# Kernel tuning notes

Measured on AMD Instinct MI355X. Metric: run time of the kernel, lower is better.

Reference implementation:

```python
import jax, jax.numpy as jnp
import numpy as np

GRID = 10
C_IN = 4          # input_dim // (grid*grid) = 400 // 100
HID = 128         # lstm hidden_dim
NV = 6            # num_vehicles
PH = 10           # pred_horizon
BN_EPS = 1e-5


def setup_inputs() -> dict:
    key = jax.random.key(0)
    ks = jax.random.split(key, 20)
    def n(k, shape, scale=0.05):
        return jax.random.normal(k, shape, jnp.float32) * scale
    return {
        "observations": jax.random.normal(ks[0], (1024, 32, 400), jnp.float32),
        # CNN
        "conv1_w": n(ks[1], (16, C_IN, 3, 3)), "conv1_b": n(ks[2], (16,)),
        "conv2_w": n(ks[3], (32, 16, 3, 3)), "conv2_b": n(ks[4], (32,)),
        # FCN (BatchNorm in eval mode: running stats + affine)
        "fc1_w": n(ks[5], (128, 128)), "fc1_b": n(ks[6], (128,)),
        "bn1_gamma": jnp.ones((128,), jnp.float32), "bn1_beta": jnp.zeros((128,), jnp.float32),
        "bn1_mean": jnp.zeros((128,), jnp.float32), "bn1_var": jnp.ones((128,), jnp.float32),
        "fc2_w": n(ks[7], (64, 128)), "fc2_b": n(ks[8], (64,)),
        "bn2_gamma": jnp.ones((64,), jnp.float32), "bn2_beta": jnp.zeros((64,), jnp.float32),
        "bn2_mean": jnp.zeros((64,), jnp.float32), "bn2_var": jnp.ones((64,), jnp.float32),
        # encoder LSTM (torch gate order i,f,g,o; b = b_ih + b_hh fused)
        "enc_w_ih": n(ks[9], (4 * HID, 64)), "enc_w_hh": n(ks[10], (4 * HID, HID)),
        "enc_b": n(ks[11], (4 * HID,)),
        # decoder LSTM
        "dec_w_ih": n(ks[12], (4 * HID, HID)), "dec_w_hh": n(ks[13], (4 * HID, HID)),
        "dec_b": n(ks[14], (4 * HID,)),
        # output head
        "out_w": n(ks[15], (2 * NV, HID)), "out_b": n(ks[16], (2 * NV,)),
    }


def _conv(x, w, b):
    y = jax.lax.conv_general_dilated(x, w, (1, 1), "SAME",
                                     dimension_numbers=("NCHW", "OIHW", "NCHW"))
    return y + b[None, :, None, None]


def _maxpool2(x):
    # MaxPool2d(2,2) with floor (drops odd trailing row/col) == VALID
    return jax.lax.reduce_window(x, -jnp.inf, jax.lax.max, (1, 1, 2, 2), (1, 1, 2, 2), "VALID")


def _bn(x, g, b, m, v):
    return (x - m) * jax.lax.rsqrt(v + BN_EPS) * g + b


def _lstm_cell(x, h, c, w_ih, w_hh, b):
    gates = x @ w_ih.T + h @ w_hh.T + b
    i, f, g, o = jnp.split(gates, 4, axis=-1)
    c_new = jax.nn.sigmoid(f) * c + jax.nn.sigmoid(i) * jnp.tanh(g)
    h_new = jax.nn.sigmoid(o) * jnp.tanh(c_new)
    return h_new, c_new


def reference(observations, conv1_w, conv1_b, conv2_w, conv2_b,
              fc1_w, fc1_b, bn1_gamma, bn1_beta, bn1_mean, bn1_var,
              fc2_w, fc2_b, bn2_gamma, bn2_beta, bn2_mean, bn2_var,
              enc_w_ih, enc_w_hh, enc_b, dec_w_ih, dec_w_hh, dec_b,
              out_w, out_b):
    B, T, D = observations.shape
    # ---- fuse the per-frame Python loop: batch all B*T frames at once ----
    x = observations.reshape(B * T, C_IN, GRID, GRID)
    x = _maxpool2(jax.nn.relu(_conv(x, conv1_w, conv1_b)))   # [BT,16,5,5]
    x = _maxpool2(jax.nn.relu(_conv(x, conv2_w, conv2_b)))   # [BT,32,2,2]
    x = x.reshape(B * T, -1)                                 # [BT,128]
    x = jax.nn.relu(_bn(x @ fc1_w.T + fc1_b, bn1_gamma, bn1_beta, bn1_mean, bn1_var))
    x = jax.nn.relu(_bn(x @ fc2_w.T + fc2_b, bn2_gamma, bn2_beta, bn2_mean, bn2_var))
    feats = x.reshape(B, T, 64)

    # ---- encoder LSTM ----
    h0 = jnp.zeros((B, HID), feats.dtype)
    c0 = jnp.zeros((B, HID), feats.dtype)
    def enc_step(carry, xt):
        h, c = carry
        h, c = _lstm_cell(xt, h, c, enc_w_ih, enc_w_hh, enc_b)
        return (h, c), h
    (h_n, c_n), hs = jax.lax.scan(enc_step, (h0, c0), jnp.swapaxes(feats, 0, 1))
    dec_x = hs[-1]  # encoder_output[:, -1]

    def dec_step(carry, _):
        x_in, h, c = carry
        h, c = _lstm_cell(x_in, h, c, dec_w_ih, dec_w_hh, dec_b)
        pred = h @ out_w.T + out_b
        return (h, h, c), pred
    _, preds = jax.lax.scan(dec_step, (dec_x, h_n, c_n), None, length=PH)
    return jnp.swapaxes(preds, 0, 1)  # [B, PH, 2*NV]
```

## Files before the change

### kernel.cpp

```cpp
#include <hip/hip_runtime.h>
#include <hip/hip_bf16.h>
#include <hip/hip_fp16.h>

constexpr int GT = 32768;
constexpr int TSEQ = 32;

typedef _Float16 h2 __attribute__((ext_vector_type(2)));

#if defined(__has_builtin)
#if __has_builtin(__builtin_amdgcn_fdot2)
#define FDOT2(a, b, c) __builtin_amdgcn_fdot2((a), (b), (c), false)
#endif
#endif
#ifndef FDOT2
#define FDOT2(a, b, c) fmaf((float)(a).x, (float)(b).x, fmaf((float)(a).y, (float)(b).y, (c)))
#endif

__device__ __forceinline__ h2 pack2(float a, float b) {
  h2 v; v.x = (_Float16)a; v.y = (_Float16)b; return v;
}

constexpr size_t OBS_T  = 0;
constexpr size_t POOL1H = 13107200;
constexpr size_t POOL2H = 0;
constexpr size_t Y1H    = 2097152;
constexpr size_t FEATSH = 19660800;
constexpr size_t GX     = 0;
constexpr size_t WB     = 26214400;
constexpr size_t W_C1   = WB + 0;
constexpr size_t W_C2H  = WB + 576;
constexpr size_t W_F1H  = WB + 2880;
constexpr size_t B_F1   = WB + 11072;
constexpr size_t W_F2H  = WB + 11200;
constexpr size_t B_F2   = WB + 15296;
constexpr size_t W_ENCXH= WB + 15360;
constexpr size_t W_ENCHH= WB + 31744;
constexpr size_t B_ENC  = WB + 64512;
constexpr size_t W_DECH = WB + 65024;
constexpr size_t B_DEC  = WB + 97792;

__device__ __forceinline__ float sigf(float x)  { return 1.f / (1.f + __expf(-x)); }
__device__ __forceinline__ float tanhfast(float x) { return 1.f - 2.f / (__expf(2.f * x) + 1.f); }

__global__ __launch_bounds__(256) void k_setup(
    const float* __restrict__ c1w, const float* __restrict__ c2w,
    const float* __restrict__ f1w, const float* __restrict__ f1b,
    const float* __restrict__ g1, const float* __restrict__ be1,
    const float* __restrict__ m1, const float* __restrict__ v1,
    const float* __restrict__ f2w, const float* __restrict__ f2b,
    const float* __restrict__ g2, const float* __restrict__ be2,
    const float* __restrict__ m2, const float* __restrict__ v2,
    const float* __restrict__ ewih, const float* __restrict__ ewhh, const float* __restrict__ eb,
    const float* __restrict__ dwih, const float* __restrict__ dwhh, const float* __restrict__ db,
    float* __restrict__ ws) {
  h2* wsh = (h2*)ws;
  long i = (long)blockIdx.x * 256 + threadIdx.x;
  if (i < 576)  { int c = i & 15, r = i >> 4; ws[W_C1 + i] = c1w[c * 36 + r]; return; }
  i -= 576;
  if (i < 2304) { int co = i & 31, q = i >> 5; int ci2 = q / 9, t9 = q % 9;
    wsh[W_C2H + i] = pack2(c2w[co * 144 + (2 * ci2) * 9 + t9],
                           c2w[co * 144 + (2 * ci2 + 1) * 9 + t9]); return; }
  i -= 2304;
  if (i < 8192) { int j = i & 127, q = i >> 7; int co2 = q >> 2, pos = q & 3;
    float s = g1[j] * rsqrtf(v1[j] + 1e-5f);
    wsh[W_F1H + i] = pack2(f1w[j * 128 + 8 * co2 + pos] * s,
                           f1w[j * 128 + 8 * co2 + 4 + pos] * s); return; }
  i -= 8192;
  if (i < 128) { int j = i; float s = g1[j] * rsqrtf(v1[j] + 1e-5f);
    ws[B_F1 + i] = (f1b[j] - m1[j]) * s + be1[j]; return; }
  i -= 128;
  if (i < 4096) { int j = i & 63, k2 = i >> 6;
    float s = g2[j] * rsqrtf(v2[j] + 1e-5f);
    wsh[W_F2H + i] = pack2(f2w[j * 128 + 2 * k2] * s,
                           f2w[j * 128 + 2 * k2 + 1] * s); return; }
  i -= 4096;
  if (i < 64) { int j = i; float s = g2[j] * rsqrtf(v2[j] + 1e-5f);
    ws[B_F2 + i] = (f2b[j] - m2[j]) * s + be2[j]; return; }
  i -= 64;
  if (i < 16384) { int r = i & 511, k2 = i >> 9;
    int u = r >> 2, gt = r & 3, jr = gt * 128 + u;
    wsh[W_ENCXH + i] = pack2(ewih[jr * 64 + 2 * k2], ewih[jr * 64 + 2 * k2 + 1]); return; }
  i -= 16384;
  if (i < 32768) { int r = i & 511, k2 = i >> 9;
    int u = r >> 2, gt = r & 3, jr = gt * 128 + u;
    wsh[W_ENCHH + i] = pack2(ewhh[jr * 128 + 2 * k2], ewhh[jr * 128 + 2 * k2 + 1]); return; }
  i -= 32768;
  if (i < 512) { int u = i >> 2, gt = i & 3; ws[B_ENC + i] = eb[gt * 128 + u]; return; }
  i -= 512;
  if (i < 32768) { int r = i & 511, k2 = i >> 9;
    int u = r >> 2, gt = r & 3, jr = gt * 128 + u;
    wsh[W_DECH + i] = pack2(dwih[jr * 128 + 2 * k2] + dwhh[jr * 128 + 2 * k2],
                            dwih[jr * 128 + 2 * k2 + 1] + dwhh[jr * 128 + 2 * k2 + 1]); return; }
  i -= 32768;
  if (i < 512) { int u = i >> 2, gt = i & 3; ws[B_DEC + i] = db[gt * 128 + u]; return; }
}

__global__ __launch_bounds__(256) void k_transpose(const float* __restrict__ obs,
                                                   float* __restrict__ obsT) {
  __shared__ float tile[64][65];
  int tp0 = blockIdx.x * 64;
  int b0  = blockIdx.y * 64;
  int q     = threadIdx.x & 15;
  int rbase = threadIdx.x >> 4;
  #pragma unroll
  for (int rr = 0; rr < 4; ++rr) {
    int row = rbase + rr * 16;
    const float4 v = *(const float4*)(obs + (size_t)(b0 + row) * 12800 + tp0 + q * 4);
    tile[row][q * 4 + 0] = v.x;
    tile[row][q * 4 + 1] = v.y;
    tile[row][q * 4 + 2] = v.z;
    tile[row][q * 4 + 3] = v.w;
  }
  __syncthreads();
  int lane = threadIdx.x & 63;
  int grp  = threadIdx.x >> 6;
  for (int cc = 0; cc < 16; ++cc) {
    int col = grp * 16 + cc;
    int tp = tp0 + col;
    int t = tp / 400, p = tp % 400;
    obsT[(size_t)p * GT + t * 1024 + b0 + lane] = tile[lane][col];
  }
}

__global__ __launch_bounds__(256) void k_conv1(const float* __restrict__ obsT,
                                               const float* __restrict__ wT,
                                               const float* __restrict__ bias,
                                               h2* __restrict__ pool1h) {
  int g = blockIdx.x * 256 + threadIdx.x;
  int pos = blockIdx.y;
  int py = pos / 5, px = pos % 5;
  float acc[4][16];
  #pragma unroll
  for (int s = 0; s < 4; ++s)
    #pragma unroll
    for (int c = 0; c < 16; ++c) acc[s][c] = 0.f;

  #pragma unroll 1
  for (int ci = 0; ci < 4; ++ci) {
    float p[16];
    #pragma unroll
    for (int r = 0; r < 4; ++r) {
      int iy = 2 * py + r - 1;
      #pragma unroll
      for (int cx = 0; cx < 4; ++cx) {
        int ix = 2 * px + cx - 1;
        bool ok = ((unsigned)iy < 10u) && ((unsigned)ix < 10u);
        p[r * 4 + cx] = ok ? obsT[(size_t)(ci * 100 + iy * 10 + ix) * GT + g] : 0.f;
      }
    }
    #pragma unroll
    for (int t9 = 0; t9 < 9; ++t9) {
      int ky = t9 / 3, kx = t9 % 3;
      const float* w = wT + ((ci * 9 + t9) << 4);
      float wv[16];
      #pragma unroll
      for (int c = 0; c < 16; ++c) wv[c] = w[c];
      #pragma unroll
      for (int dy = 0; dy < 2; ++dy)
        #pragma unroll
        for (int dx = 0; dx < 2; ++dx) {
          float xv = p[(dy + ky) * 4 + (dx + kx)];
          #pragma unroll
          for (int c = 0; c < 16; ++c)
            acc[dy * 2 + dx][c] = fmaf(wv[c], xv, acc[dy * 2 + dx][c]);
        }
    }
  }
  float m[16];
  #pragma unroll
  for (int c = 0; c < 16; ++c) {
    float v = fmaxf(fmaxf(acc[0][c], acc[1][c]), fmaxf(acc[2][c], acc[3][c]));
    m[c] = fmaxf(v + bias[c], 0.f);
  }
  #pragma unroll
  for (int c2 = 0; c2 < 8; ++c2)
    pool1h[(size_t)(c2 * 25 + pos) * GT + g] = pack2(m[2 * c2], m[2 * c2 + 1]);
}

__global__ __launch_bounds__(256) void k_conv2h(const h2* __restrict__ pool1h,
                                                const h2* __restrict__ wch,
                                                const float* __restrict__ bias,
                                                h2* __restrict__ pool2h) {
  int g = blockIdx.x * 256 + threadIdx.x;
  int pos = blockIdx.y & 3;
  int h = blockIdx.y >> 2;
  int py = pos >> 1, px = pos & 1;
  float acc[4][8];
  #pragma unroll
  for (int s = 0; s < 4; ++s)
    #pragma unroll
    for (int c = 0; c < 8; ++c) acc[s][c] = 0.f;
  const h2 hz = pack2(0.f, 0.f);

  #pragma unroll 1
  for (int ci2 = 0; ci2 < 8; ++ci2) {
    h2 p[16];
    #pragma unroll
    for (int r = 0; r < 4; ++r) {
      int iy = 2 * py + r - 1;
      #pragma unroll
      for (int cx = 0; cx < 4; ++cx) {
        int ix = 2 * px + cx - 1;
        bool ok = ((unsigned)iy < 5u) && ((unsigned)ix < 5u);
        p[r * 4 + cx] = ok ? pool1h[(size_t)(ci2 * 25 + iy * 5 + ix) * GT + g] : hz;
      }
    }
    #pragma unroll
    for (int t9 = 0; t9 < 9; ++t9) {
      int ky = t9 / 3, kx = t9 % 3;
      const h2* w = wch + (ci2 * 9 + t9) * 32 + h * 8;
      h2 wv[8];
      #pragma unroll
      for (int c = 0; c < 8; ++c) wv[c] = w[c];
      #pragma unroll
      for (int dy = 0; dy < 2; ++dy)
        #pragma unroll
        for (int dx = 0; dx < 2; ++dx) {
          h2 xv = p[(dy + ky) * 4 + (dx + kx)];
          #pragma unroll
          for (int c = 0; c < 8; ++c)
            acc[dy * 2 + dx][c] = FDOT2(xv, wv[c], acc[dy * 2 + dx][c]);
        }
    }
  }
  float m[8];
  #pragma unroll
  for (int c = 0; c < 8; ++c) {
    float v = fmaxf(fmaxf(acc[0][c], acc[1][c]), fmaxf(acc[2][c], acc[3][c]));
    m[c] = fmaxf(v + bias[h * 8 + c], 0.f);
  }
  #pragma unroll
  for (int c2 = 0; c2 < 4; ++c2) {
    int q = (h * 4 + c2) * 4 + pos;
    pool2h[(size_t)q * GT + g] = pack2(m[2 * c2], m[2 * c2 + 1]);
  }
}

__global__ __launch_bounds__(256) void k_fc16h(const h2* __restrict__ x,
                                               const h2* __restrict__ WT,
                                               const float* __restrict__ bf,
                                               h2* __restrict__ y, int K2, int J) {
  int g = blockIdx.x * 256 + threadIdx.x;
  int j0 = blockIdx.y * 16;
  float acc[16];
  #pragma unroll
  for (int c = 0; c < 16; ++c) acc[c] = 0.f;
  for (int k2 = 0; k2 < K2; ++k2) {
    h2 xv = x[(size_t)k2 * GT + g];
    const h2* w = WT + (size_t)k2 * J + j0;
    #pragma unroll
    for (int c = 0; c < 16; ++c) acc[c] = FDOT2(xv, w[c], acc[c]);
  }
  #pragma unroll
  for (int c2 = 0; c2 < 8; ++c2) {
    float a = fmaxf(acc[2 * c2] + bf[j0 + 2 * c2], 0.f);
    float b = fmaxf(acc[2 * c2 + 1] + bf[j0 + 2 * c2 + 1], 0.f);
    y[(size_t)(j0 / 2 + c2) * GT + g] = pack2(a, b);
  }
}

__global__ __launch_bounds__(256) void k_xgatesh(const h2* __restrict__ featsh,
                                                 const h2* __restrict__ wxh,
                                                 const float* __restrict__ br,
                                                 float* __restrict__ gx) {
  int t  = blockIdx.x >> 2;
  int bq = blockIdx.x & 3;
  int b  = bq * 256 + threadIdx.x;
  int r0 = blockIdx.y * 32;
  float acc[32];
  #pragma unroll
  for (int i = 0; i < 32; ++i) acc[i] = br[r0 + i];
  const h2* xcol = featsh + (size_t)t * 1024 + b;
  for (int k2 = 0; k2 < 32; ++k2) {
    h2 xv = xcol[(size_t)k2 * GT];
    const h2* w = wxh + k2 * 512 + r0;
    #pragma unroll
    for (int i = 0; i < 32; ++i) acc[i] = FDOT2(xv, w[i], acc[i]);
  }
  float* gxs = gx + (size_t)t * 524288 + (size_t)b * 512 + r0;
  #pragma unroll
  for (int i = 0; i < 32; ++i) gxs[i] = acc[i];
}

__global__ __launch_bounds__(512, 2) void k_seq8(
    const float* __restrict__ gx,
    const h2* __restrict__ WENCH, const h2* __restrict__ WDECH,
    const float* __restrict__ bdec,
    const float* __restrict__ ow, const float* __restrict__ ob,
    float* __restrict__ out) {
  const int tid = threadIdx.x;
  const int bl2 = tid & 1;
  const int kg  = (tid >> 1) & 1;
  const int g   = tid >> 2;
  const int b0  = blockIdx.x * 4 + bl2 * 2;

  __shared__ h2 hbufh[2][4 * 68];
  __shared__ h2 owl2[12 * 68];

  for (int i = tid; i < 2 * 4 * 68; i += 512) ((h2*)hbufh)[i] = pack2(0.f, 0.f);
  for (int i = tid; i < 768; i += 512) {
    int o = i >> 6, k2 = i & 63;
    owl2[o * 68 + k2] = pack2(ow[o * 128 + 2 * k2], ow[o * 128 + 2 * k2 + 1]);
  }
  const float obv = (tid < 48) ? ob[tid >> 2] : 0.f;

  h2 wreg[32][4];
  #pragma unroll
  for (int p = 0; p < 32; ++p)
    *(uint4*)wreg[p] = *(const uint4*)(WENCH + (size_t)(kg * 32 + p) * 512 + g * 4);

  float c0 = 0.f, c1 = 0.f;
  __syncthreads();
  int cur = 0;

  for (int t = 0; t < TSEQ; ++t) {
    const float4 ga = *(const float4*)(gx + (size_t)t * 524288 + (size_t)b0 * 512 + g * 4);
    const float4 gb = *(const float4*)(gx + (size_t)t * 524288 + (size_t)(b0 + 1) * 512 + g * 4);

    float acc[8];
    #pragma unroll
    for (int r = 0; r < 8; ++r) acc[r] = 0.f;

    #pragma unroll
    for (int b = 0; b < 2; ++b) {
      const h2* hp = &hbufh[cur][(bl2 * 2 + b) * 68 + kg * 32];
      #pragma unroll
      for (int pc = 0; pc < 8; ++pc) {
        h2 hh[4];
        *(uint4*)hh = *(const uint4*)&hp[pc * 4];
        #pragma unroll
        for (int j = 0; j < 4; ++j) {
          const int p = pc * 4 + j;
          acc[b * 4 + 0] = FDOT2(hh[j], wreg[p][0], acc[b * 4 + 0]);
          acc[b * 4 + 1] = FDOT2(hh[j], wreg[p][1], acc[b * 4 + 1]);
          acc[b * 4 + 2] = FDOT2(hh[j], wreg[p][2], acc[b * 4 + 2]);
          acc[b * 4 + 3] = FDOT2(hh[j], wreg[p][3], acc[b * 4 + 3]);
        }
      }
    }
    float D[8];
    #pragma unroll
    for (int r = 0; r < 8; ++r) D[r] = acc[r] + __shfl_xor(acc[r], 2, 64);

    const float gi0 = D[0] + ga.x, gf0 = D[1] + ga.y, gg0 = D[2] + ga.z, go0 = D[3] + ga.w;
    const float gi1 = D[4] + gb.x, gf1 = D[5] + gb.y, gg1 = D[6] + gb.z, go1 = D[7] + gb.w;
    c0 = sigf(gf0) * c0 + sigf(gi0) * tanhfast(gg0);
    c1 = sigf(gf1) * c1 + sigf(gi1) * tanhfast(gg1);
    const float hn0 = sigf(go0) * tanhfast(c0);
    const float hn1 = sigf(go1) * tanhfast(c1);
    if (kg == 0) {
      _Float16* hf = (_Float16*)&hbufh[cur ^ 1][0];
      hf[(bl2 * 2 + 0) * 136 + g] = (_Float16)hn0;
      hf[(bl2 * 2 + 1) * 136 + g] = (_Float16)hn1;
    }
    __syncthreads();
    cur ^= 1;
  }

  #pragma unroll
  for (int p = 0; p < 32; ++p)
    *(uint4*)wreg[p] = *(const uint4*)(WDECH + (size_t)(kg * 32 + p) * 512 + g * 4);
  const float4 bd = *(const float4*)(bdec + g * 4);

  for (int t = 0; t < 10; ++t) {
    float acc[8];
    #pragma unroll
    for (int r = 0; r < 8; ++r) acc[r] = 0.f;

    #pragma unroll
    for (int b = 0; b < 2; ++b) {
      const h2* hp = &hbufh[cur][(bl2 * 2 + b) * 68 + kg * 32];
      #pragma unroll
      for (int pc = 0; pc < 8; ++pc) {
        h2 hh[4];
        *(uint4*)hh = *(const uint4*)&hp[pc * 4];
        #pragma unroll
        for (int j = 0; j < 4; ++j) {
          const int p = pc * 4 + j;
          acc[b * 4 + 0] = FDOT2(hh[j], wreg[p][0], acc[b * 4 + 0]);
          acc[b * 4 + 1] = FDOT2(hh[j], wreg[p][1], acc[b * 4 + 1]);
          acc[b * 4 + 2] = FDOT2(hh[j], wreg[p][2], acc[b * 4 + 2]);
          acc[b * 4 + 3] = FDOT2(hh[j], wreg[p][3], acc[b * 4 + 3]);
        }
      }
    }
    float D[8];
    #pragma unroll
    for (int r = 0; r < 8; ++r) D[r] = acc[r] + __shfl_xor(acc[r], 2, 64);

    const float gi0 = D[0] + bd.x, gf0 = D[1] + bd.y, gg0 = D[2] + bd.z, go0 = D[3] + bd.w;
    const float gi1 = D[4] + bd.x, gf1 = D[5] + bd.y, gg1 = D[6] + bd.z, go1 = D[7] + bd.w;
    c0 = sigf(gf0) * c0 + sigf(gi0) * tanhfast(gg0);
    c1 = sigf(gf1) * c1 + sigf(gi1) * tanhfast(gg1);
    const float hn0 = sigf(go0) * tanhfast(c0);
    const float hn1 = sigf(go1) * tanhfast(c1);
    if (kg == 0) {
      _Float16* hf = (_Float16*)&hbufh[cur ^ 1][0];
      hf[(bl2 * 2 + 0) * 136 + g] = (_Float16)hn0;
      hf[(bl2 * 2 + 1) * 136 + g] = (_Float16)hn1;
    }
    __syncthreads();
    cur ^= 1;
    if (tid < 48) {
      const int o  = tid >> 2;
      const int bh = tid & 3;
      const h2* hh = &hbufh[cur][bh * 68];
      const h2* wo = &owl2[o * 68];
      float oacc = obv;
      #pragma unroll
      for (int k2 = 0; k2 < 64; ++k2) oacc = FDOT2(hh[k2], wo[k2], oacc);
      out[(blockIdx.x * 4 + bh) * 120 + t * 12 + o] = oacc;
    }
  }
}

extern "C" void kernel_launch(void* const* d_in, const int* in_sizes, int n_in,
                              void* d_out, int out_size, void* d_ws, size_t ws_size,
                              hipStream_t stream) {
  const float* obs  = (const float*)d_in[0];
  const float* c1w  = (const float*)d_in[1];
  const float* c1b  = (const float*)d_in[2];
  const float* c2w  = (const float*)d_in[3];
  const float* c2b  = (const float*)d_in[4];
  const float* f1w  = (const float*)d_in[5];
  const float* f1b  = (const float*)d_in[6];
  const float* g1   = (const float*)d_in[7];
  const float* be1  = (const float*)d_in[8];
  const float* m1   = (const float*)d_in[9];
  const float* v1   = (const float*)d_in[10];
  const float* f2w  = (const float*)d_in[11];
  const float* f2b  = (const float*)d_in[12];
  const float* g2   = (const float*)d_in[13];
  const float* be2  = (const float*)d_in[14];
  const float* m2   = (const float*)d_in[15];
  const float* v2   = (const float*)d_in[16];
  const float* ewih = (const float*)d_in[17];
  const float* ewhh = (const float*)d_in[18];
  const float* eb   = (const float*)d_in[19];
  const float* dwih = (const float*)d_in[20];
  const float* dwhh = (const float*)d_in[21];
  const float* db   = (const float*)d_in[22];
  const float* ow   = (const float*)d_in[23];
  const float* ob   = (const float*)d_in[24];
  float* ws  = (float*)d_ws;
  h2*    wsh = (h2*)d_ws;
  float* out = (float*)d_out;

  k_setup<<<384, 256, 0, stream>>>(c1w, c2w, f1w, f1b, g1, be1, m1, v1,
                                   f2w, f2b, g2, be2, m2, v2,
                                   ewih, ewhh, eb, dwih, dwhh, db, ws);
  k_transpose<<<dim3(200, 16), 256, 0, stream>>>(obs, ws + OBS_T);
  k_conv1<<<dim3(128, 25), 256, 0, stream>>>(ws + OBS_T, ws + W_C1, c1b, wsh + POOL1H);
  k_conv2h<<<dim3(128, 16), 256, 0, stream>>>(wsh + POOL1H, wsh + W_C2H, c2b, wsh + POOL2H);
  k_fc16h<<<dim3(128, 8), 256, 0, stream>>>(wsh + POOL2H, wsh + W_F1H, ws + B_F1,
                                            wsh + Y1H, 64, 128);
  k_fc16h<<<dim3(128, 4), 256, 0, stream>>>(wsh + Y1H, wsh + W_F2H, ws + B_F2,
                                            wsh + FEATSH, 64, 64);
  k_xgatesh<<<dim3(128, 16), 256, 0, stream>>>(wsh + FEATSH, wsh + W_ENCXH, ws + B_ENC,
                                               ws + GX);
  k_seq8<<<256, 512, 0, stream>>>(ws + GX, wsh + W_ENCHH, wsh + W_DECH,
                                  ws + B_DEC, ow, ob, out);
}
```

Baseline: 381.9 us.

## Fuse conv2, fc1 and fc2 into one kernel; widen and coalesce xgates output

Merges conv2+pool, fc1+BN+ReLU and fc2+BN+ReLU into a single kernel. The intermediate pooled and fc1 activations stay in shared memory instead of round-tripping through global memory, and three launches are removed. The xgates kernel now computes 64 gate rows per thread with vectorized weight loads, then stages results through shared memory for coalesced float4 stores. The cost is heavier register and LDS use per block, which may lower occupancy, and fewer blocks in the fused stage.

```diff
diff --git a/kernel.cpp b/kernel.cpp
--- a/kernel.cpp
+++ b/kernel.cpp
@@ -22,8 +22,6 @@
 
 constexpr size_t OBS_T  = 0;
 constexpr size_t POOL1H = 13107200;
-constexpr size_t POOL2H = 0;
-constexpr size_t Y1H    = 2097152;
 constexpr size_t FEATSH = 19660800;
 constexpr size_t GX     = 0;
 constexpr size_t WB     = 26214400;
@@ -177,109 +175,171 @@
     pool1h[(size_t)(c2 * 25 + pos) * GT + g] = pack2(m[2 * c2], m[2 * c2 + 1]);
 }
 
-__global__ __launch_bounds__(256) void k_conv2h(const h2* __restrict__ pool1h,
-                                                const h2* __restrict__ wch,
-                                                const float* __restrict__ bias,
-                                                h2* __restrict__ pool2h) {
-  int g = blockIdx.x * 256 + threadIdx.x;
-  int pos = blockIdx.y & 3;
-  int h = blockIdx.y >> 2;
-  int py = pos >> 1, px = pos & 1;
-  float acc[4][8];
-  #pragma unroll
-  for (int s = 0; s < 4; ++s)
-    #pragma unroll
-    for (int c = 0; c < 8; ++c) acc[s][c] = 0.f;
+__global__ __launch_bounds__(256, 2) void k_cfx(
+    const h2* __restrict__ pool1h,
+    const h2* __restrict__ wc2, const float* __restrict__ c2b,
+    const h2* __restrict__ wf1, const float* __restrict__ bf1,
+    const h2* __restrict__ wf2, const float* __restrict__ bf2,
+    h2* __restrict__ featsh) {
+  const int tid = threadIdx.x;
+  const int fr  = tid & 63;
+  const int sl  = tid >> 6;
+  const int g   = blockIdx.x * 64 + fr;
+
+  __shared__ h2 xbuf[64 * 68];
+  __shared__ h2 y1buf[64 * 68];
+
+  const int py = sl >> 1, px = sl & 1;
   const h2 hz = pack2(0.f, 0.f);
-
   #pragma unroll 1
-  for (int ci2 = 0; ci2 < 8; ++ci2) {
-    h2 p[16];
-    #pragma unroll
-    for (int r = 0; r < 4; ++r) {
-      int iy = 2 * py + r - 1;
-      #pragma unroll
-      for (int cx = 0; cx < 4; ++cx) {
-        int ix = 2 * px + cx - 1;
-        bool ok = ((unsigned)iy < 5u) && ((unsigned)ix < 5u);
-        p[r * 4 + cx] = ok ? pool1h[(size_t)(ci2 * 25 + iy * 5 + ix) * GT + g] : hz;
+  for (int ho = 0; ho < 2; ++ho) {
+    float acc[4][16];
+    #pragma unroll
+    for (int s = 0; s < 4; ++s)
+      #pragma unroll
+      for (int c = 0; c < 16; ++c) acc[s][c] = 0.f;
+
+    #pragma unroll 1
+    for (int ci2 = 0; ci2 < 8; ++ci2) {
+      h2 p[16];
+      #pragma unroll
+      for (int r = 0; r < 4; ++r) {
+        int iy = 2 * py + r - 1;
+        #pragma unroll
+        for (int cx = 0; cx < 4; ++cx) {
+          int ix = 2 * px + cx - 1;
+          bool ok = ((unsigned)iy < 5u) && ((unsigned)ix < 5u);
+          p[r * 4 + cx] = ok ? pool1h[(size_t)(ci2 * 25 + iy * 5 + ix) * GT + g] : hz;
+        }
       }
-    }
-    #pragma unroll
-    for (int t9 = 0; t9 < 9; ++t9) {
-      int ky = t9 / 3, kx = t9 % 3;
-      const h2* w = wch + (ci2 * 9 + t9) * 32 + h * 8;
-      h2 wv[8];
-      #pragma unroll
-      for (int c = 0; c < 8; ++c) wv[c] = w[c];
-      #pragma unroll
-      for (int dy = 0; dy < 2; ++dy)
+      #pragma unroll
+      for (int t9 = 0; t9 < 9; ++t9) {
+        int ky = t9 / 3, kx = t9 % 3;
+        const h2* w = wc2 + (ci2 * 9 + t9) * 32 + ho * 16;
+        h2 wv[16];
         #pragma unroll
-        for (int dx = 0; dx < 2; ++dx) {
-          h2 xv = p[(dy + ky) * 4 + (dx + kx)];
+        for (int u = 0; u < 4; ++u) *(uint4*)&wv[u * 4] = *(const uint4*)&w[u * 4];
+        #pragma unroll
+        for (int dy = 0; dy < 2; ++dy)
           #pragma unroll
-          for (int c = 0; c < 8; ++c)
-            acc[dy * 2 + dx][c] = FDOT2(xv, wv[c], acc[dy * 2 + dx][c]);
-        }
-    }
-  }
-  float m[8];
-  #pragma unroll
-  for (int c = 0; c < 8; ++c) {
-    float v = fmaxf(fmaxf(acc[0][c], acc[1][c]), fmaxf(acc[2][c], acc[3][c]));
-    m[c] = fmaxf(v + bias[h * 8 + c], 0.f);
-  }
-  #pragma unroll
-  for (int c2 = 0; c2 < 4; ++c2) {
-    int q = (h * 4 + c2) * 4 + pos;
-    pool2h[(size_t)q * GT + g] = pack2(m[2 * c2], m[2 * c2 + 1]);
-  }
-}
-
-__global__ __launch_bounds__(256) void k_fc16h(const h2* __restrict__ x,
-                                               const h2* __restrict__ WT,
-                                               const float* __restrict__ bf,
-                                               h2* __restrict__ y, int K2, int J) {
-  int g = blockIdx.x * 256 + threadIdx.x;
-  int j0 = blockIdx.y * 16;
-  float acc[16];
-  #pragma unroll
-  for (int c = 0; c < 16; ++c) acc[c] = 0.f;
-  for (int k2 = 0; k2 < K2; ++k2) {
-    h2 xv = x[(size_t)k2 * GT + g];
-    const h2* w = WT + (size_t)k2 * J + j0;
-    #pragma unroll
-    for (int c = 0; c < 16; ++c) acc[c] = FDOT2(xv, w[c], acc[c]);
-  }
-  #pragma unroll
-  for (int c2 = 0; c2 < 8; ++c2) {
-    float a = fmaxf(acc[2 * c2] + bf[j0 + 2 * c2], 0.f);
-    float b = fmaxf(acc[2 * c2 + 1] + bf[j0 + 2 * c2 + 1], 0.f);
-    y[(size_t)(j0 / 2 + c2) * GT + g] = pack2(a, b);
-  }
-}
-
-__global__ __launch_bounds__(256) void k_xgatesh(const h2* __restrict__ featsh,
-                                                 const h2* __restrict__ wxh,
-                                                 const float* __restrict__ br,
-                                                 float* __restrict__ gx) {
+          for (int dx = 0; dx < 2; ++dx) {
+            h2 xv = p[(dy + ky) * 4 + (dx + kx)];
+            #pragma unroll
+            for (int c = 0; c < 16; ++c)
+              acc[dy * 2 + dx][c] = FDOT2(xv, wv[c], acc[dy * 2 + dx][c]);
+          }
+      }
+    }
+    #pragma unroll
+    for (int c2 = 0; c2 < 8; ++c2) {
+      float va = fmaxf(fmaxf(acc[0][2 * c2], acc[1][2 * c2]),
+                       fmaxf(acc[2][2 * c2], acc[3][2 * c2]));
+      float vb = fmaxf(fmaxf(acc[0][2 * c2 + 1], acc[1][2 * c2 + 1]),
+                       fmaxf(acc[2][2 * c2 + 1], acc[3][2 * c2 + 1]));
+      float a = fmaxf(va + c2b[ho * 16 + 2 * c2], 0.f);
+      float b = fmaxf(vb + c2b[ho * 16 + 2 * c2 + 1], 0.f);
+      int q = (ho * 8 + c2) * 4 + sl;
+      xbuf[fr * 68 + q] = pack2(a, b);
+    }
+  }
+  __syncthreads();
+
+  h2 x[64];
+  #pragma unroll
+  for (int k = 0; k < 16; ++k)
+    *(uint4*)&x[k * 4] = *(const uint4*)&xbuf[fr * 68 + k * 4];
+
+  {
+    float acc1[32];
+    #pragma unroll
+    for (int c = 0; c < 32; ++c) acc1[c] = 0.f;
+    #pragma unroll 1
+    for (int q = 0; q < 64; ++q) {
+      const h2* w = wf1 + q * 128 + sl * 32;
+      h2 wv[32];
+      #pragma unroll
+      for (int u = 0; u < 8; ++u) *(uint4*)&wv[u * 4] = *(const uint4*)&w[u * 4];
+      h2 xv = x[q];
+      #pragma unroll
+      for (int c = 0; c < 32; ++c) acc1[c] = FDOT2(xv, wv[c], acc1[c]);
+    }
+    const int j0 = sl * 32;
+    #pragma unroll
+    for (int c2 = 0; c2 < 16; ++c2) {
+      float a = fmaxf(acc1[2 * c2] + bf1[j0 + 2 * c2], 0.f);
+      float b = fmaxf(acc1[2 * c2 + 1] + bf1[j0 + 2 * c2 + 1], 0.f);
+      y1buf[fr * 68 + sl * 16 + c2] = pack2(a, b);
+    }
+  }
+  __syncthreads();
+
+  #pragma unroll
+  for (int k = 0; k < 16; ++k)
+    *(uint4*)&x[k * 4] = *(const uint4*)&y1buf[fr * 68 + k * 4];
+
+  {
+    float acc2[16];
+    #pragma unroll
+    for (int c = 0; c < 16; ++c) acc2[c] = 0.f;
+    #pragma unroll 1
+    for (int k2 = 0; k2 < 64; ++k2) {
+      const h2* w = wf2 + k2 * 64 + sl * 16;
+      h2 wv[16];
+      #pragma unroll
+      for (int u = 0; u < 4; ++u) *(uint4*)&wv[u * 4] = *(const uint4*)&w[u * 4];
+      h2 xv = x[k2];
+      #pragma unroll
+      for (int c = 0; c < 16; ++c) acc2[c] = FDOT2(xv, wv[c], acc2[c]);
+    }
+    const int j0 = sl * 16;
+    #pragma unroll
+    for (int c2 = 0; c2 < 8; ++c2) {
+      float a = fmaxf(acc2[2 * c2] + bf2[j0 + 2 * c2], 0.f);
+      float b = fmaxf(acc2[2 * c2 + 1] + bf2[j0 + 2 * c2 + 1], 0.f);
+      featsh[(size_t)(sl * 8 + c2) * GT + g] = pack2(a, b);
+    }
+  }
+}
+
+__global__ __launch_bounds__(256, 2) void k_xgatesh(const h2* __restrict__ featsh,
+                                                    const h2* __restrict__ wxh,
+                                                    const float* __restrict__ br,
+                                                    float* __restrict__ gx) {
+  __shared__ float lbuf[256 * 68];
   int t  = blockIdx.x >> 2;
   int bq = blockIdx.x & 3;
   int b  = bq * 256 + threadIdx.x;
-  int r0 = blockIdx.y * 32;
-  float acc[32];
-  #pragma unroll
-  for (int i = 0; i < 32; ++i) acc[i] = br[r0 + i];
+  int r0 = blockIdx.y * 64;
+  float acc[64];
+  #pragma unroll
+  for (int i = 0; i < 64; ++i) acc[i] = br[r0 + i];
   const h2* xcol = featsh + (size_t)t * 1024 + b;
+  #pragma unroll 1
   for (int k2 = 0; k2 < 32; ++k2) {
     h2 xv = xcol[(size_t)k2 * GT];
     const h2* w = wxh + k2 * 512 + r0;
-    #pragma unroll
-    for (int i = 0; i < 32; ++i) acc[i] = FDOT2(xv, w[i], acc[i]);
-  }
-  float* gxs = gx + (size_t)t * 524288 + (size_t)b * 512 + r0;
-  #pragma unroll
-  for (int i = 0; i < 32; ++i) gxs[i] = acc[i];
+    h2 wv[64];
+    #pragma unroll
+    for (int u = 0; u < 16; ++u) *(uint4*)&wv[u * 4] = *(const uint4*)&w[u * 4];
+    #pragma unroll
+    for (int i = 0; i < 64; ++i) acc[i] = FDOT2(xv, wv[i], acc[i]);
+  }
+  float* lp = lbuf + threadIdx.x * 68;
+  #pragma unroll
+  for (int u = 0; u < 16; ++u) {
+    float4 v = make_float4(acc[4 * u], acc[4 * u + 1], acc[4 * u + 2], acc[4 * u + 3]);
+    *(float4*)&lp[u * 4] = v;
+  }
+  __syncthreads();
+  const int r4 = threadIdx.x & 15;
+  const int bb = threadIdx.x >> 4;
+  const size_t base = (size_t)t * 524288 + (size_t)(bq * 256) * 512 + r0;
+  #pragma unroll
+  for (int j = 0; j < 16; ++j) {
+    int bl = j * 16 + bb;
+    float4 v = *(const float4*)&lbuf[bl * 68 + r4 * 4];
+    *(float4*)&gx[base + (size_t)bl * 512 + r4 * 4] = v;
+  }
 }
 
 __global__ __launch_bounds__(512, 2) void k_seq8(
@@ -451,13 +511,11 @@
                                    ewih, ewhh, eb, dwih, dwhh, db, ws);
   k_transpose<<<dim3(200, 16), 256, 0, stream>>>(obs, ws + OBS_T);
   k_conv1<<<dim3(128, 25), 256, 0, stream>>>(ws + OBS_T, ws + W_C1, c1b, wsh + POOL1H);
-  k_conv2h<<<dim3(128, 16), 256, 0, stream>>>(wsh + POOL1H, wsh + W_C2H, c2b, wsh + POOL2H);
-  k_fc16h<<<dim3(128, 8), 256, 0, stream>>>(wsh + POOL2H, wsh + W_F1H, ws + B_F1,
-                                            wsh + Y1H, 64, 128);
-  k_fc16h<<<dim3(128, 4), 256, 0, stream>>>(wsh + Y1H, wsh + W_F2H, ws + B_F2,
-                                            wsh + FEATSH, 64, 64);
-  k_xgatesh<<<dim3(128, 16), 256, 0, stream>>>(wsh + FEATSH, wsh + W_ENCXH, ws + B_ENC,
-                                               ws + GX);
+  k_cfx<<<512, 256, 0, stream>>>(wsh + POOL1H, wsh + W_C2H, c2b,
+                                 wsh + W_F1H, ws + B_F1,
+                                 wsh + W_F2H, ws + B_F2, wsh + FEATSH);
+  k_xgatesh<<<dim3(128, 8), 256, 0, stream>>>(wsh + FEATSH, wsh + W_ENCXH, ws + B_ENC,
+                                              ws + GX);
   k_seq8<<<256, 512, 0, stream>>>(ws + GX, wsh + W_ENCHH, wsh + W_DECH,
                                   ws + B_DEC, ow, ob, out);
 }
```

Result: slower. 421.8 us (+10.4%).
